# Optimization experiments

Measured on AMD Instinct MI355X. Metric: run time of the kernel, lower is better.

The kernel has to match this reference:

```python
import jax, jax.numpy as jnp
import numpy as np

B, U, D_DEC, D_ENC = 32, 4096, 512, 512
ATT_UNITS, NUM_HEADS = 512, 4
HEAD_DIM = ATT_UNITS // NUM_HEADS
CONV_FILTERS, CONV_K = 32, 31
INIT = 0.075


def setup_inputs() -> dict:
    key = jax.random.key(0)
    ks = jax.random.split(key, 12)
    u = lambda k, shape: jax.random.uniform(k, shape, jnp.float32, -INIT, INIT)
    return {
        "dec_state": jax.random.normal(ks[0], (B, D_DEC), jnp.float32),
        "enc_state": jax.random.normal(ks[1], (B, U, D_ENC), jnp.float32),
        "prev_attention_weights": jax.random.uniform(ks[2], (B, U), jnp.float32),
        # stacked per-head Dense params
        "Wphi": u(ks[3], (NUM_HEADS, D_DEC, HEAD_DIM)),
        "bphi": jnp.zeros((NUM_HEADS, HEAD_DIM), jnp.float32),
        "Wpsi": u(ks[4], (NUM_HEADS, D_ENC, HEAD_DIM)),
        "bpsi": jnp.zeros((NUM_HEADS, HEAD_DIM), jnp.float32),
        # Conv1D kernel in WIO layout: (kernel_size, in_ch=1, out_ch=32), no bias
        "conv_kernel": jax.random.uniform(ks[5], (CONV_K, 1, CONV_FILTERS), jnp.float32, -0.1, 0.1),
        "Wloc": u(ks[6], (CONV_FILTERS, NUM_HEADS)),
        "Wout": u(ks[7], (NUM_HEADS * D_ENC, ATT_UNITS)),
        "bout": jnp.zeros((ATT_UNITS,), jnp.float32),
    }


def reference(dec_state, enc_state, prev_attention_weights,
              Wphi, bphi, Wpsi, bpsi, conv_kernel, Wloc, Wout, bout):
    # location features: Conv1D(same, no bias) over prev attention weights
    loc_feat = jax.lax.conv_general_dilated(
        prev_attention_weights[:, :, None], conv_kernel,
        window_strides=(1,), padding="SAME",
        dimension_numbers=("NWC", "WIO", "NWC"))            # (B, U, 32)
    loc_bias = loc_feat @ Wloc                                 # (B, U, H)
    loc_bias = jnp.transpose(loc_bias, (0, 2, 1))              # (B, H, U)

    # batched per-head projections (replaces the Python per-head loop)
    phi_s = jnp.einsum("bd,hdk->bhk", dec_state, Wphi) + bphi          # (B, H, hd)
    psi_h = jnp.einsum("bue,hek->bhuk", enc_state, Wpsi) + bpsi[:, None, :]  # (B, H, U, hd)

    energy = jnp.einsum("bhk,bhuk->bhu", phi_s, psi_h) + loc_bias      # (B, H, U)
    attn = jax.nn.softmax(energy, axis=-1)                              # (B, H, U)

    context = jnp.einsum("bhu,bue->bhe", attn, enc_state)               # (B, H, E)
    combined = context.reshape(context.shape[0], -1)                    # (B, H*E)
    context_vector = combined @ Wout + bout                             # (B, ATT_UNITS)
    attention_weights = jnp.mean(attn, axis=1)                          # (B, U)
    return context_vector, attention_weights
```

## Files before the change

kernel.cpp:

```cpp
#include <hip/hip_runtime.h>
#include <math.h>

#define B  32
#define U  4096
#define D  512
#define H  4
#define HD 128
#define CK 31
#define CF 32
#define AU 512

#define BPB    32
#define ROWS_W 32

#define LOG2E 1.4426950408889634f

static __device__ __forceinline__ float readlane_f(float v, int l) {
    return __int_as_float(__builtin_amdgcn_readlane(__float_as_int(v), l));
}
static __device__ __forceinline__ float fast_exp2(float x) {
    return __builtin_amdgcn_exp2f(x);
}

__global__ __launch_bounds__(256) void prep_kernel(
    const float* __restrict__ dec,
    const float* __restrict__ Wphi,
    const float* __restrict__ bphi,
    const float* __restrict__ Wpsi,
    const float* __restrict__ bpsi,
    const float* __restrict__ convk,
    const float* __restrict__ Wloc,
    float* __restrict__ ws_v,
    float* __restrict__ ws_const,
    float* __restrict__ ws_ck,
    float* __restrict__ outv)
{
    __shared__ float decs[D];
    __shared__ float phis2[2][HD];
    __shared__ float phis[HD];
    const int b = blockIdx.x / H, h = blockIdx.x % H;
    const int tid = threadIdx.x;

    if (tid < 128) outv[(size_t)b * AU + h * 128 + tid] = 0.f;

    for (int i = tid; i < D; i += 256) decs[i] = dec[b * D + i];
    __syncthreads();

    {
        const int k = tid & 127, half = tid >> 7;
        const int d0 = half * 256;
        float acc = 0.f;
        const float* wp = Wphi + (size_t)h * D * HD + (size_t)d0 * HD + k;
        #pragma unroll 8
        for (int d = 0; d < 256; ++d) acc += decs[d0 + d] * wp[(size_t)d * HD];
        phis2[half][k] = acc;
    }
    __syncthreads();
    if (tid < HD) phis[tid] = phis2[0][tid] + phis2[1][tid] + bphi[h * HD + tid];
    __syncthreads();

    if (tid == 0) {
        float c = 0.f;
        for (int k = 0; k < HD; ++k) c += phis[k] * bpsi[h * HD + k];
        ws_const[b * H + h] = c * LOG2E;
    }

    for (int e = tid; e < D; e += 256) {
        const float4* wq = (const float4*)(Wpsi + ((size_t)h * D + e) * HD);
        float acc = 0.f;
        #pragma unroll 8
        for (int k = 0; k < HD / 4; ++k) {
            float4 w = wq[k];
            acc += w.x * phis[4*k] + w.y * phis[4*k+1]
                 + w.z * phis[4*k+2] + w.w * phis[4*k+3];
        }
        ws_v[((size_t)b * H + h) * D + e] = acc * LOG2E;
    }

    if (blockIdx.x == 0 && tid < CK * H) {
        int t = tid / H, hh = tid % H;
        float acc = 0.f;
        for (int f = 0; f < CF; ++f) acc += convk[t * CF + f] * Wloc[f * H + hh];
        ws_ck[t * H + hh] = acc * LOG2E;
    }
}

__global__ __launch_bounds__(256, 4) void fused_pass1(
    const float* __restrict__ enc,
    const float* __restrict__ prevw,
    const float* __restrict__ ws_v,
    const float* __restrict__ ws_const,
    const float* __restrict__ ws_ck,
    float* __restrict__ energy,
    float* __restrict__ pctx,
    float* __restrict__ pms)
{
    const int b    = blockIdx.y;
    const int blk  = blockIdx.x;
    const int tid  = threadIdx.x;
    const int lane = tid & 63;
    const int wave = tid >> 6;
    const int ubase = (blk * 4 + wave) * ROWS_W;

    __shared__ float lctx[4][H][D];
    __shared__ float lms[4][H][2];
    __shared__ float lalpha[H][4];

    float4 v0[H], v1[H];
    #pragma unroll
    for (int h = 0; h < H; ++h) {
        const float* vp = ws_v + ((size_t)b * H + h) * D;
        v0[h] = *(const float4*)(vp + lane * 4);
        v1[h] = *(const float4*)(vp + 256 + lane * 4);
    }
    float ckr[H] = {0.f, 0.f, 0.f, 0.f};
    if (lane < CK) {
        #pragma unroll
        for (int h = 0; h < H; ++h) ckr[h] = ws_ck[lane * H + h];
    }
    float ct[H];
    #pragma unroll
    for (int h = 0; h < H; ++h) ct[h] = ws_const[b * H + h];

    float w0;
    {
        const int gi = ubase - 15 + lane;
        w0 = (gi >= 0 && gi < U) ? prevw[b * U + gi] : 0.f;
    }

    float m0 = -3.402823466e38f, m1 = m0, m2 = m0, m3 = m0;
    float s0 = 0.f, s1 = 0.f, s2 = 0.f, s3 = 0.f;
    float4 z = {0.f, 0.f, 0.f, 0.f};
    float4 c00 = z, c01 = z, c10 = z, c11 = z, c20 = z, c21 = z, c30 = z, c31 = z;

    const bool b16 = (lane & 16) != 0;
    const bool b32 = (lane & 32) != 0;

    const float* encb = enc + ((size_t)b * U + ubase) * D;
    float4 e0 = *(const float4*)(encb + lane * 4);
    float4 e1 = *(const float4*)(encb + 256 + lane * 4);

    for (int r = 0; r < ROWS_W; ++r) {
        float4 n0, n1;
        if (r < ROWS_W - 1) {
            const float* nx = encb + (size_t)(r + 1) * D;
            n0 = *(const float4*)(nx + lane * 4);
            n1 = *(const float4*)(nx + 256 + lane * 4);
        }
        const int u = ubase + r;
        float pw = __int_as_float(
            __builtin_amdgcn_ds_bpermute((r + lane) << 2, __float_as_int(w0)));

        float p0 = pw * ckr[0]
            + e0.x*v0[0].x + e0.y*v0[0].y + e0.z*v0[0].z + e0.w*v0[0].w
            + e1.x*v1[0].x + e1.y*v1[0].y + e1.z*v1[0].z + e1.w*v1[0].w;
        float p1 = pw * ckr[1]
            + e0.x*v0[1].x + e0.y*v0[1].y + e0.z*v0[1].z + e0.w*v0[1].w
            + e1.x*v1[1].x + e1.y*v1[1].y + e1.z*v1[1].z + e1.w*v1[1].w;
        float p2 = pw * ckr[2]
            + e0.x*v0[2].x + e0.y*v0[2].y + e0.z*v0[2].z + e0.w*v0[2].w
            + e1.x*v1[2].x + e1.y*v1[2].y + e1.z*v1[2].z + e1.w*v1[2].w;
        float p3 = pw * ckr[3]
            + e0.x*v0[3].x + e0.y*v0[3].y + e0.z*v0[3].z + e0.w*v0[3].w
            + e1.x*v1[3].x + e1.y*v1[3].y + e1.z*v1[3].z + e1.w*v1[3].w;

        float keepA = b16 ? p1 : p0, sendA = b16 ? p0 : p1;
        float a  = keepA + __shfl_xor(sendA, 16);
        float keepB = b16 ? p3 : p2, sendB = b16 ? p2 : p3;
        float bb = keepB + __shfl_xor(sendB, 16);
        float keepC = b32 ? bb : a, sendC = b32 ? a : bb;
        float c = keepC + __shfl_xor(sendC, 32);
        c += __shfl_xor(c, 1);
        c += __shfl_xor(c, 2);
        c += __shfl_xor(c, 4);
        c += __shfl_xor(c, 8);
        float eh0 = readlane_f(c, 0)  + ct[0];
        float eh1 = readlane_f(c, 16) + ct[1];
        float eh2 = readlane_f(c, 32) + ct[2];
        float eh3 = readlane_f(c, 48) + ct[3];

        if (lane < H) {
            float ev = (lane == 0) ? eh0 : (lane == 1) ? eh1 : (lane == 2) ? eh2 : eh3;
            energy[((size_t)b * H + lane) * U + u] = ev;
        }

        float mn0 = fmaxf(m0, eh0), mn1 = fmaxf(m1, eh1);
        float mn2 = fmaxf(m2, eh2), mn3 = fmaxf(m3, eh3);
        if (mn0 > m0 || mn1 > m1 || mn2 > m2 || mn3 > m3) {
            float a0 = fast_exp2(m0 - mn0), a1 = fast_exp2(m1 - mn1);
            float a2 = fast_exp2(m2 - mn2), a3 = fast_exp2(m3 - mn3);
            s0 *= a0; s1 *= a1; s2 *= a2; s3 *= a3;
            c00.x*=a0; c00.y*=a0; c00.z*=a0; c00.w*=a0; c01.x*=a0; c01.y*=a0; c01.z*=a0; c01.w*=a0;
            c10.x*=a1; c10.y*=a1; c10.z*=a1; c10.w*=a1; c11.x*=a1; c11.y*=a1; c11.z*=a1; c11.w*=a1;
            c20.x*=a2; c20.y*=a2; c20.z*=a2; c20.w*=a2; c21.x*=a2; c21.y*=a2; c21.z*=a2; c21.w*=a2;
            c30.x*=a3; c30.y*=a3; c30.z*=a3; c30.w*=a3; c31.x*=a3; c31.y*=a3; c31.z*=a3; c31.w*=a3;
            m0 = mn0; m1 = mn1; m2 = mn2; m3 = mn3;
        }
        float w0e = fast_exp2(eh0 - m0), w1e = fast_exp2(eh1 - m1);
        float w2e = fast_exp2(eh2 - m2), w3e = fast_exp2(eh3 - m3);
        s0 += w0e; s1 += w1e; s2 += w2e; s3 += w3e;
        c00.x += w0e*e0.x; c00.y += w0e*e0.y; c00.z += w0e*e0.z; c00.w += w0e*e0.w;
        c01.x += w0e*e1.x; c01.y += w0e*e1.y; c01.z += w0e*e1.z; c01.w += w0e*e1.w;
        c10.x += w1e*e0.x; c10.y += w1e*e0.y; c10.z += w1e*e0.z; c10.w += w1e*e0.w;
        c11.x += w1e*e1.x; c11.y += w1e*e1.y; c11.z += w1e*e1.z; c11.w += w1e*e1.w;
        c20.x += w2e*e0.x; c20.y += w2e*e0.y; c20.z += w2e*e0.z; c20.w += w2e*e0.w;
        c21.x += w2e*e1.x; c21.y += w2e*e1.y; c21.z += w2e*e1.z; c21.w += w2e*e1.w;
        c30.x += w3e*e0.x; c30.y += w3e*e0.y; c30.z += w3e*e0.z; c30.w += w3e*e0.w;
        c31.x += w3e*e1.x; c31.y += w3e*e1.y; c31.z += w3e*e1.z; c31.w += w3e*e1.w;

        e0 = n0; e1 = n1;
    }

    *(float4*)&lctx[wave][0][lane * 4]       = c00;
    *(float4*)&lctx[wave][0][256 + lane * 4] = c01;
    *(float4*)&lctx[wave][1][lane * 4]       = c10;
    *(float4*)&lctx[wave][1][256 + lane * 4] = c11;
    *(float4*)&lctx[wave][2][lane * 4]       = c20;
    *(float4*)&lctx[wave][2][256 + lane * 4] = c21;
    *(float4*)&lctx[wave][3][lane * 4]       = c30;
    *(float4*)&lctx[wave][3][256 + lane * 4] = c31;
    if (lane == 0) {
        lms[wave][0][0] = m0; lms[wave][0][1] = s0;
        lms[wave][1][0] = m1; lms[wave][1][1] = s1;
        lms[wave][2][0] = m2; lms[wave][2][1] = s2;
        lms[wave][3][0] = m3; lms[wave][3][1] = s3;
    }
    __syncthreads();

    const size_t pbase = ((size_t)(b * BPB + blk)) * H;
    if (tid < H) {
        const int h = tid;
        float M = fmaxf(fmaxf(lms[0][h][0], lms[1][h][0]),
                        fmaxf(lms[2][h][0], lms[3][h][0]));
        float S = 0.f;
        #pragma unroll
        for (int w = 0; w < 4; ++w) {
            float al = fast_exp2(lms[w][h][0] - M);
            lalpha[h][w] = al;
            S += al * lms[w][h][1];
        }
        pms[(pbase + h) * 2]     = M;
        pms[(pbase + h) * 2 + 1] = S;
    }
    __syncthreads();

    #pragma unroll
    for (int h = 0; h < H; ++h) {
        const float a0 = lalpha[h][0], a1 = lalpha[h][1];
        const float a2 = lalpha[h][2], a3 = lalpha[h][3];
        #pragma unroll
        for (int half = 0; half < 2; ++half) {
            const int d = tid + half * 256;
            float val = a0 * lctx[0][h][d] + a1 * lctx[1][h][d]
                      + a2 * lctx[2][h][d] + a3 * lctx[3][h][d];
            pctx[(pbase + h) * D + d] = val;
        }
    }
}

__global__ __launch_bounds__(256) void combine_kernel(
    const float* __restrict__ pctx,
    const float* __restrict__ pms,
    float* __restrict__ ctx,
    float* __restrict__ MS)
{
    const int bh = blockIdx.x;
    const int b = bh >> 2, h = bh & 3;
    const int tid = threadIdx.x;
    __shared__ float sm[BPB], ss[BPB], salpha[BPB];
    __shared__ float MSsh[2];

    if (tid < BPB) {
        sm[tid] = pms[(((size_t)b * BPB + tid) * H + h) * 2];
        ss[tid] = pms[(((size_t)b * BPB + tid) * H + h) * 2 + 1];
    }
    __syncthreads();
    if (tid == 0) {
        float M = -3.402823466e38f;
        for (int i = 0; i < BPB; ++i) M = fmaxf(M, sm[i]);
        float S = 0.f;
        for (int i = 0; i < BPB; ++i) {
            float al = fast_exp2(sm[i] - M);
            salpha[i] = al;
            S += al * ss[i];
        }
        MSsh[0] = M; MSsh[1] = S;
        MS[bh * 2] = M; MS[bh * 2 + 1] = S;
    }
    __syncthreads();
    const float invS = 1.0f / MSsh[1];

    float acc0 = 0.f, acc1 = 0.f;
    const float* base = pctx + ((size_t)b * BPB * H + h) * D;
    #pragma unroll 4
    for (int i = 0; i < BPB; ++i) {
        float al = salpha[i];
        const float* p = base + (size_t)i * H * D;
        acc0 += al * p[tid];
        acc1 += al * p[tid + 256];
    }
    ctx[(size_t)bh * D + tid]       = acc0 * invS;
    ctx[(size_t)bh * D + tid + 256] = acc1 * invS;
}

__global__ __launch_bounds__(256) void tail_kernel(
    const float* __restrict__ energy,
    const float* __restrict__ MS,
    const float* __restrict__ ctx,
    const float* __restrict__ Wout,
    const float* __restrict__ bout,
    float* __restrict__ attw,
    float* __restrict__ outv)
{
    const int b = blockIdx.x;
    const int role = blockIdx.y;
    const int tid = threadIdx.x;

    if (role < 16) {
        const int u = role * 256 + tid;
        float acc = 0.f;
        #pragma unroll
        for (int h = 0; h < H; ++h) {
            const float M  = MS[(b * H + h) * 2];
            const float iS = 1.0f / MS[(b * H + h) * 2 + 1];
            acc += fast_exp2(energy[((size_t)b * H + h) * U + u] - M) * iS;
        }
        attw[(size_t)b * U + u] = acc * 0.25f;
    } else {
        const int idx = role - 16;
        const int jh  = idx & 1;
        const int kc  = idx >> 1;
        const int j   = jh * 256 + tid;
        const int i0  = kc * 256;
        __shared__ float c_s[256];
        c_s[tid] = ctx[(size_t)b * (H * D) + i0 + tid];
        __syncthreads();

        float acc = (kc == 0) ? bout[j] : 0.f;
        #pragma unroll 8
        for (int i = 0; i < 256; ++i)
            acc += c_s[i] * Wout[(size_t)(i0 + i) * AU + j];
        atomicAdd(&outv[(size_t)b * AU + j], acc);
    }
}

extern "C" void kernel_launch(void* const* d_in, const int* in_sizes, int n_in,
                              void* d_out, int out_size, void* d_ws, size_t ws_size,
                              hipStream_t stream) {
    const float* dec   = (const float*)d_in[0];
    const float* enc   = (const float*)d_in[1];
    const float* prevw = (const float*)d_in[2];
    const float* Wphi  = (const float*)d_in[3];
    const float* bphi  = (const float*)d_in[4];
    const float* Wpsi  = (const float*)d_in[5];
    const float* bpsi  = (const float*)d_in[6];
    const float* convk = (const float*)d_in[7];
    const float* Wloc  = (const float*)d_in[8];
    const float* Wout  = (const float*)d_in[9];
    const float* bout  = (const float*)d_in[10];

    float* out  = (float*)d_out;
    float* outv = out;
    float* attw = out + B * AU;

    float* ws        = (float*)d_ws;
    float* ws_v      = ws;
    float* ws_const  = ws + 65536;
    float* ws_ck     = ws + 65664;
    float* ws_energy = ws + 65792;
    float* ws_pctx   = ws_energy + (size_t)B*H*U;
    float* ws_pms    = ws_pctx + (size_t)B*BPB*H*D;
    float* ws_MS     = ws_pms + (size_t)B*BPB*H*2;
    float* ws_ctx    = ws_MS + 256;

    prep_kernel<<<dim3(B * H), 256, 0, stream>>>(dec, Wphi, bphi, Wpsi, bpsi,
                                                 convk, Wloc, ws_v, ws_const,
                                                 ws_ck, outv);
    fused_pass1<<<dim3(BPB, B), 256, 0, stream>>>(enc, prevw, ws_v, ws_const,
                                                  ws_ck, ws_energy, ws_pctx, ws_pms);
    combine_kernel<<<dim3(B * H), 256, 0, stream>>>(ws_pctx, ws_pms, ws_ctx, ws_MS);
    tail_kernel<<<dim3(B, 32), 256, 0, stream>>>(ws_energy, ws_MS, ws_ctx,
                                                 Wout, bout, attw, outv);
}
```

Before: 429.7 us.

## Fold split-softmax combine into tail kernel and vectorize phi projection

Removes the separate combine kernel. The tail kernel blocks now each recompute the per-head max and sum from the partial stats, and the Wout blocks rebuild their own 256-element context slice from the partial contexts. This saves one launch and the round trip of the ctx and MS buffers, at the cost of redundant small reductions in every block. Separately, the phi projection in prep now uses float4 loads across 8 depth groups, which adds an extra shared-memory reduction.

```diff
diff --git a/kernel.cpp b/kernel.cpp
--- a/kernel.cpp
+++ b/kernel.cpp
@@ -36,7 +36,7 @@
     float* __restrict__ outv)
 {
     __shared__ float decs[D];
-    __shared__ float phis2[2][HD];
+    __shared__ float ph8[8][HD];
     __shared__ float phis[HD];
     const int b = blockIdx.x / H, h = blockIdx.x % H;
     const int tid = threadIdx.x;
@@ -47,16 +47,26 @@
     __syncthreads();
 
     {
-        const int k = tid & 127, half = tid >> 7;
-        const int d0 = half * 256;
-        float acc = 0.f;
-        const float* wp = Wphi + (size_t)h * D * HD + (size_t)d0 * HD + k;
+        const int kq = (tid & 31) * 4;
+        const int dg = tid >> 5;
+        float4 acc = {0.f, 0.f, 0.f, 0.f};
+        const float* wp = Wphi + (size_t)h * D * HD + (size_t)dg * HD + kq;
         #pragma unroll 8
-        for (int d = 0; d < 256; ++d) acc += decs[d0 + d] * wp[(size_t)d * HD];
-        phis2[half][k] = acc;
-    }
-    __syncthreads();
-    if (tid < HD) phis[tid] = phis2[0][tid] + phis2[1][tid] + bphi[h * HD + tid];
+        for (int d0 = 0; d0 < D; d0 += 8) {
+            float dv = decs[d0 + dg];
+            float4 w = *(const float4*)(wp + (size_t)d0 * HD);
+            acc.x += dv * w.x; acc.y += dv * w.y;
+            acc.z += dv * w.z; acc.w += dv * w.w;
+        }
+        *(float4*)&ph8[dg][kq] = acc;
+    }
+    __syncthreads();
+    if (tid < HD) {
+        float s = ph8[0][tid] + ph8[1][tid] + ph8[2][tid] + ph8[3][tid]
+                + ph8[4][tid] + ph8[5][tid] + ph8[6][tid] + ph8[7][tid]
+                + bphi[h * HD + tid];
+        phis[tid] = s;
+    }
     __syncthreads();
 
     if (tid == 0) {
@@ -258,55 +268,10 @@
     }
 }
 
-__global__ __launch_bounds__(256) void combine_kernel(
-    const float* __restrict__ pctx,
-    const float* __restrict__ pms,
-    float* __restrict__ ctx,
-    float* __restrict__ MS)
-{
-    const int bh = blockIdx.x;
-    const int b = bh >> 2, h = bh & 3;
-    const int tid = threadIdx.x;
-    __shared__ float sm[BPB], ss[BPB], salpha[BPB];
-    __shared__ float MSsh[2];
-
-    if (tid < BPB) {
-        sm[tid] = pms[(((size_t)b * BPB + tid) * H + h) * 2];
-        ss[tid] = pms[(((size_t)b * BPB + tid) * H + h) * 2 + 1];
-    }
-    __syncthreads();
-    if (tid == 0) {
-        float M = -3.402823466e38f;
-        for (int i = 0; i < BPB; ++i) M = fmaxf(M, sm[i]);
-        float S = 0.f;
-        for (int i = 0; i < BPB; ++i) {
-            float al = fast_exp2(sm[i] - M);
-            salpha[i] = al;
-            S += al * ss[i];
-        }
-        MSsh[0] = M; MSsh[1] = S;
-        MS[bh * 2] = M; MS[bh * 2 + 1] = S;
-    }
-    __syncthreads();
-    const float invS = 1.0f / MSsh[1];
-
-    float acc0 = 0.f, acc1 = 0.f;
-    const float* base = pctx + ((size_t)b * BPB * H + h) * D;
-    #pragma unroll 4
-    for (int i = 0; i < BPB; ++i) {
-        float al = salpha[i];
-        const float* p = base + (size_t)i * H * D;
-        acc0 += al * p[tid];
-        acc1 += al * p[tid + 256];
-    }
-    ctx[(size_t)bh * D + tid]       = acc0 * invS;
-    ctx[(size_t)bh * D + tid + 256] = acc1 * invS;
-}
-
 __global__ __launch_bounds__(256) void tail_kernel(
     const float* __restrict__ energy,
-    const float* __restrict__ MS,
-    const float* __restrict__ ctx,
+    const float* __restrict__ pms,
+    const float* __restrict__ pctx,
     const float* __restrict__ Wout,
     const float* __restrict__ bout,
     float* __restrict__ attw,
@@ -317,30 +282,72 @@
     const int tid = threadIdx.x;
 
     if (role < 16) {
+        __shared__ float lsm[H][BPB], lss[H][BPB];
+        __shared__ float lM[H], liS[H];
+        if (tid < 128) {
+            const int k = tid >> 2, h = tid & 3;
+            lsm[h][k] = pms[(((size_t)b * BPB + k) * H + h) * 2];
+            lss[h][k] = pms[(((size_t)b * BPB + k) * H + h) * 2 + 1];
+        }
+        __syncthreads();
+        if (tid < H) {
+            float M = -3.402823466e38f;
+            for (int i = 0; i < BPB; ++i) M = fmaxf(M, lsm[tid][i]);
+            float S = 0.f;
+            for (int i = 0; i < BPB; ++i)
+                S += fast_exp2(lsm[tid][i] - M) * lss[tid][i];
+            lM[tid] = M; liS[tid] = 1.0f / S;
+        }
+        __syncthreads();
+
         const int u = role * 256 + tid;
         float acc = 0.f;
         #pragma unroll
-        for (int h = 0; h < H; ++h) {
-            const float M  = MS[(b * H + h) * 2];
-            const float iS = 1.0f / MS[(b * H + h) * 2 + 1];
-            acc += fast_exp2(energy[((size_t)b * H + h) * U + u] - M) * iS;
-        }
+        for (int h = 0; h < H; ++h)
+            acc += fast_exp2(energy[((size_t)b * H + h) * U + u] - lM[h]) * liS[h];
         attw[(size_t)b * U + u] = acc * 0.25f;
     } else {
         const int idx = role - 16;
         const int jh  = idx & 1;
         const int kc  = idx >> 1;
+        const int h   = kc >> 1;
+        const int e0  = (kc & 1) * 256;
         const int j   = jh * 256 + tid;
-        const int i0  = kc * 256;
+
+        __shared__ float lsm2[BPB], lss2[BPB], sal[BPB];
+        __shared__ float sinv;
         __shared__ float c_s[256];
-        c_s[tid] = ctx[(size_t)b * (H * D) + i0 + tid];
-        __syncthreads();
-
-        float acc = (kc == 0) ? bout[j] : 0.f;
+
+        if (tid < BPB) {
+            lsm2[tid] = pms[(((size_t)b * BPB + tid) * H + h) * 2];
+            lss2[tid] = pms[(((size_t)b * BPB + tid) * H + h) * 2 + 1];
+        }
+        __syncthreads();
+        if (tid == 0) {
+            float M = -3.402823466e38f;
+            for (int i = 0; i < BPB; ++i) M = fmaxf(M, lsm2[i]);
+            float S = 0.f;
+            for (int i = 0; i < BPB; ++i) {
+                float al = fast_exp2(lsm2[i] - M);
+                sal[i] = al;
+                S += al * lss2[i];
+            }
+            sinv = 1.0f / S;
+        }
+        __syncthreads();
+
+        float acc = 0.f;
+        const float* pp = pctx + (((size_t)b * BPB) * H + h) * D + e0 + tid;
+        #pragma unroll 8
+        for (int k = 0; k < BPB; ++k) acc += sal[k] * pp[(size_t)k * H * D];
+        c_s[tid] = acc * sinv;
+        __syncthreads();
+
+        float o = (kc == 0) ? bout[j] : 0.f;
         #pragma unroll 8
         for (int i = 0; i < 256; ++i)
-            acc += c_s[i] * Wout[(size_t)(i0 + i) * AU + j];
-        atomicAdd(&outv[(size_t)b * AU + j], acc);
+            o += c_s[i] * Wout[(size_t)(kc * 256 + i) * AU + j];
+        atomicAdd(&outv[(size_t)b * AU + j], o);
     }
 }
 
@@ -370,15 +377,12 @@
     float* ws_energy = ws + 65792;
     float* ws_pctx   = ws_energy + (size_t)B*H*U;
     float* ws_pms    = ws_pctx + (size_t)B*BPB*H*D;
-    float* ws_MS     = ws_pms + (size_t)B*BPB*H*2;
-    float* ws_ctx    = ws_MS + 256;
 
     prep_kernel<<<dim3(B * H), 256, 0, stream>>>(dec, Wphi, bphi, Wpsi, bpsi,
                                                  convk, Wloc, ws_v, ws_const,
                                                  ws_ck, outv);
     fused_pass1<<<dim3(BPB, B), 256, 0, stream>>>(enc, prevw, ws_v, ws_const,
                                                   ws_ck, ws_energy, ws_pctx, ws_pms);
-    combine_kernel<<<dim3(B * H), 256, 0, stream>>>(ws_pctx, ws_pms, ws_ctx, ws_MS);
-    tail_kernel<<<dim3(B, 32), 256, 0, stream>>>(ws_energy, ws_MS, ws_ctx,
+    tail_kernel<<<dim3(B, 32), 256, 0, stream>>>(ws_energy, ws_pms, ws_pctx,
                                                  Wout, bout, attw, outv);
 }
```

New measurement: 416.9 us. 1.03x faster.
